# Kernel optimization log

Measured on AMD Instinct MI355X. Metric: run time of the kernel, lower is better.

## Reference

```python
import jax, jax.numpy as jnp
import numpy as np

B, L, C, H, W = 2, 16, 16, 64, 64


def setup_inputs() -> dict:
    key = jax.random.key(0)
    k1, k2 = jax.random.split(key)
    # flows scaled so cumulative normalized-coordinate flows mostly stay in [-1, 1]
    flows = jax.random.normal(k1, (B, L, 2, H, W), dtype=jnp.float32) * 0.05
    images = jax.random.normal(k2, (B, L, C, H, W), dtype=jnp.float32)
    return {"flows": flows, "images": images}


def _bilinear_sample(images, gx, gy):
    # images: [B, Lj, C, H, W]; gx, gy: [B, Li, Lj, H, W] normalized coords in [-1, 1]
    # Replicates torch.nn.functional.grid_sample(mode='bilinear',
    # padding_mode='zeros', align_corners=False).
    Bs, Lj, Cs, Hs, Ws = images.shape
    ix = ((gx + 1.0) * Ws - 1.0) * 0.5  # pixel x coord
    iy = ((gy + 1.0) * Hs - 1.0) * 0.5  # pixel y coord
    x0f = jnp.floor(ix)
    y0f = jnp.floor(iy)
    wx = ix - x0f  # weight toward x0+1 (differentiable w.r.t. flow)
    wy = iy - y0f
    x0 = x0f.astype(jnp.int32)
    y0 = y0f.astype(jnp.int32)
    img_flat = images.reshape(Bs, Lj, Cs, Hs * Ws)

    def gather(xi, yi):
        valid = (xi >= 0) & (xi < Ws) & (yi >= 0) & (yi < Hs)  # [B,Li,Lj,H,W]
        lin = jnp.clip(yi, 0, Hs - 1) * Ws + jnp.clip(xi, 0, Ws - 1)
        lin_t = jnp.transpose(lin, (0, 2, 1, 3, 4))  # [B,Lj,Li,H,W]
        # per (b, j): gather [C, HW] at indices [Li, H, W] -> [C, Li, H, W]
        v = jax.vmap(jax.vmap(lambda im, l: im[:, l]))(img_flat, lin_t)
        v = jnp.transpose(v, (0, 3, 1, 2, 4, 5))  # [B,Li,Lj,C,H,W]
        return v * valid[:, :, :, None, :, :].astype(v.dtype)

    v00 = gather(x0, y0)
    v01 = gather(x0 + 1, y0)
    v10 = gather(x0, y0 + 1)
    v11 = gather(x0 + 1, y0 + 1)
    wX = wx[:, :, :, None, :, :]
    wY = wy[:, :, :, None, :, :]
    return (v00 * (1.0 - wX) * (1.0 - wY) + v01 * wX * (1.0 - wY)
            + v10 * (1.0 - wX) * wY + v11 * wX * wY)


def reference(flows, images):
    Bs, Ls, _, Hs, Ws = flows.shape
    dt = flows.dtype
    cum = jnp.cumsum(flows, axis=1)  # [B,L,2,H,W]
    # rel[b, i, j] = cum[b, i] - cum[b, j]  -> [B,Li,Lj,2,H,W]
    rel = cum[:, :, None] - cum[:, None, :]
    # base sampling grid (pixel centers in normalized coords)
    gx_base = (jnp.arange(Ws, dtype=dt) + 0.5) * (2.0 / Ws) - 1.0  # [W]
    gy_base = (jnp.arange(Hs, dtype=dt) + 0.5) * (2.0 / Hs) - 1.0  # [H]
    gx = gx_base + rel[:, :, :, 0]              # [B,Li,Lj,H,W]
    gy = gy_base[:, None] + rel[:, :, :, 1]     # [B,Li,Lj,H,W]
    gx = jnp.remainder(gx + 1.0, 2.0) - 1.0     # wrap x into [-1, 1)
    warped = _bilinear_sample(images, gx, gy)   # [B,Li,Lj,C,H,W]
    mask = jnp.tril(jnp.ones((Ls, Ls), dtype=dt))
    # causal accumulate over source index j
    return jnp.einsum('bijchw,ij->bichw', warped, mask)
```

## Files before the change

kernel.cpp:

```cpp
#include <hip/hip_runtime.h>
#include <hip/hip_fp16.h>

#define BB 2
#define LL 16
#define CC 16
#define HH 64
#define WW 64
#define HWSZ (HH * WW)

__device__ __forceinline__ float2 cvt2(unsigned int u) {
    __half2 h = *reinterpret_cast<const __half2*>(&u);
    return __half22float2(h);
}

__global__ __launch_bounds__(256) void gsp_prep(
    const float* __restrict__ images,
    uint4* __restrict__ h16)
{
    const int gid  = blockIdx.x * 256 + threadIdx.x;
    const int half = gid & 1;
    const int pix  = (gid >> 1) & (HWSZ - 1);
    const int bl   = gid >> 13;

    const float* src = images + (size_t)(bl * CC + half * 8) * HWSZ + pix;
    unsigned short hs[8];
    #pragma unroll
    for (int m = 0; m < 8; ++m) {
        __half h = __float2half(src[(size_t)m * HWSZ]);
        hs[m] = *reinterpret_cast<unsigned short*>(&h);
    }
    uint4 v;
    v.x = (unsigned)hs[0] | ((unsigned)hs[1] << 16);
    v.y = (unsigned)hs[2] | ((unsigned)hs[3] << 16);
    v.z = (unsigned)hs[4] | ((unsigned)hs[5] << 16);
    v.w = (unsigned)hs[6] | ((unsigned)hs[7] << 16);
    h16[((size_t)bl * HWSZ + pix) * 2 + half] = v;
}

__global__ __launch_bounds__(256) void gsp_main(
    const float* __restrict__ flows,
    const uint4* __restrict__ h16,
    float* __restrict__ out)
{
    const int idx  = blockIdx.x;
    const int xcd  = idx & 7;
    const int k    = idx >> 3;
    const int i    = 15 - (k >> 4);
    const int b    = (k >> 3) & 1;
    const int tile = xcd * 8 + (k & 7);

    const int sub  = threadIdx.x & 3;
    const int half = sub & 1;
    const int xc   = sub >> 1;
    const int px   = tile * 64 + (threadIdx.x >> 2);
    const int h = px >> 6;
    const int w = px & (WW - 1);

    float cx16[LL], cy16[LL];
    {
        const float* fb = flows + (size_t)b * LL * 2 * HWSZ + px;
        #pragma unroll
        for (int l = 0; l < LL; ++l) {
            cx16[l] = fb[(size_t)l * 2 * HWSZ];
            cy16[l] = fb[(size_t)l * 2 * HWSZ + HWSZ];
        }
        #pragma unroll
        for (int l = 1; l < LL; ++l) { cx16[l] += cx16[l - 1]; cy16[l] += cy16[l - 1]; }
    }

    const uint4* h16_b = h16 + (size_t)(b * LL) * HWSZ * 2;

    const float gxb = (w + 0.5f) * (2.0f / WW) - 1.0f;
    const float gyb = (h + 0.5f) * (2.0f / HH) - 1.0f;

    float cix = 0.0f, ciy = 0.0f;
    #pragma unroll
    for (int l = 0; l < LL; ++l) { if (l == i) { cix = cx16[l]; ciy = cy16[l]; } }

    float acc[8];
    #pragma unroll
    for (int m = 0; m < 8; ++m) acc[m] = 0.0f;

    #pragma unroll
    for (int j = 0; j < LL - 1; ++j) {
        if (j < i) {
            float gx = gxb + (cix - cx16[j]);
            float gy = gyb + (ciy - cy16[j]);

            float tt = gx + 1.0f;
            tt = tt - floorf(tt * 0.5f) * 2.0f;
            gx = tt - 1.0f;

            const float ix = ((gx + 1.0f) * WW - 1.0f) * 0.5f;
            const float iy = ((gy + 1.0f) * HH - 1.0f) * 0.5f;
            const float x0f = floorf(ix);
            const float y0f = floorf(iy);
            const float fx = ix - x0f;
            const float fy = iy - y0f;
            const int x0 = (int)x0f;
            const int y0 = (int)y0f;

            const int  xr = x0 + xc;
            const bool vx = (xr >= 0) && (xr < WW);
            const int  cx = min(max(xr, 0), WW - 1);
            const float wx = (xc ? fx : (1.0f - fx)) * (vx ? 1.0f : 0.0f);

            const int y1i = y0 + 1;
            const bool vy0 = (y0 >= 0) && (y0 < HH);
            const bool vy1 = (y1i >= 0) && (y1i < HH);
            const int cy0 = min(max(y0, 0), HH - 1);
            const int cy1 = min(max(y1i, 0), HH - 1);

            const uint4* jb = h16_b + (size_t)j * HWSZ * 2;
            const uint4 v0 = jb[(cy0 * WW + cx) * 2 + half];
            const uint4 v1 = jb[(cy1 * WW + cx) * 2 + half];

            const float w0 = wx * (1.0f - fy) * (vy0 ? 1.0f : 0.0f);
            const float w1 = wx * fy * (vy1 ? 1.0f : 0.0f);

            {
                const float2 p0 = cvt2(v0.x), p1 = cvt2(v0.y);
                const float2 p2 = cvt2(v0.z), p3 = cvt2(v0.w);
                acc[0] += w0 * p0.x;  acc[1] += w0 * p0.y;
                acc[2] += w0 * p1.x;  acc[3] += w0 * p1.y;
                acc[4] += w0 * p2.x;  acc[5] += w0 * p2.y;
                acc[6] += w0 * p3.x;  acc[7] += w0 * p3.y;
            }
            {
                const float2 p0 = cvt2(v1.x), p1 = cvt2(v1.y);
                const float2 p2 = cvt2(v1.z), p3 = cvt2(v1.w);
                acc[0] += w1 * p0.x;  acc[1] += w1 * p0.y;
                acc[2] += w1 * p1.x;  acc[3] += w1 * p1.y;
                acc[4] += w1 * p2.x;  acc[5] += w1 * p2.y;
                acc[6] += w1 * p3.x;  acc[7] += w1 * p3.y;
            }
        }
    }

    #pragma unroll
    for (int m = 0; m < 8; ++m) acc[m] += __shfl_xor(acc[m], 2, 64);

    float s0 = xc ? acc[4] : acc[0];
    float s1 = xc ? acc[5] : acc[1];
    float s2 = xc ? acc[6] : acc[2];
    float s3 = xc ? acc[7] : acc[3];

    {
        const uint2* h2 = (const uint2*)h16;
        const uint2 idv = h2[(((size_t)(b * LL + i) * HWSZ + px) * 2 + half) * 2 + xc];
        const float2 p0 = cvt2(idv.x), p1 = cvt2(idv.y);
        s0 += p0.x; s1 += p0.y; s2 += p1.x; s3 += p1.y;
    }

    const int q = half * 2 + xc;
    float* op = out + ((size_t)(b * LL + i) * CC + q * 4) * HWSZ + px;
    __builtin_nontemporal_store(s0, op + 0 * HWSZ);
    __builtin_nontemporal_store(s1, op + 1 * HWSZ);
    __builtin_nontemporal_store(s2, op + 2 * HWSZ);
    __builtin_nontemporal_store(s3, op + 3 * HWSZ);
}

extern "C" void kernel_launch(void* const* d_in, const int* in_sizes, int n_in,
                              void* d_out, int out_size, void* d_ws, size_t ws_size,
                              hipStream_t stream) {
    const float* flows  = (const float*)d_in[0];
    const float* images = (const float*)d_in[1];
    float* out = (float*)d_out;
    uint4* h16 = (uint4*)d_ws;

    gsp_prep<<<1024, 256, 0, stream>>>(images, h16);

    gsp_main<<<2048, 256, 0, stream>>>(flows, h16, out);
}
```

Before: 75.67 us.

## Precompute cumulative flows in prep kernel and software-pipeline gather loop

The prep kernel gains extra blocks that compute per-pixel cumulative flow sums into an interleaved workspace buffer. The main kernel stages these into swizzled shared memory instead of each thread reloading and summing 32 flow values. The unrolled predicated j-loop becomes a runtime loop that prefetches the next iteration's gathers before accumulating the current one, with launch bounds raised to 5 blocks per CU for occupancy. This trades register arrays for shared memory and a barrier, and adds workspace traffic for the cumulative buffer.

```diff
diff --git a/kernel.cpp b/kernel.cpp
--- a/kernel.cpp
+++ b/kernel.cpp
@@ -15,33 +15,104 @@
 
 __global__ __launch_bounds__(256) void gsp_prep(
     const float* __restrict__ images,
-    uint4* __restrict__ h16)
+    const float* __restrict__ flows,
+    uint4* __restrict__ h16,
+    float4* __restrict__ cum4)
 {
-    const int gid  = blockIdx.x * 256 + threadIdx.x;
-    const int half = gid & 1;
-    const int pix  = (gid >> 1) & (HWSZ - 1);
-    const int bl   = gid >> 13;
-
-    const float* src = images + (size_t)(bl * CC + half * 8) * HWSZ + pix;
-    unsigned short hs[8];
-    #pragma unroll
-    for (int m = 0; m < 8; ++m) {
-        __half h = __float2half(src[(size_t)m * HWSZ]);
-        hs[m] = *reinterpret_cast<unsigned short*>(&h);
-    }
-    uint4 v;
-    v.x = (unsigned)hs[0] | ((unsigned)hs[1] << 16);
-    v.y = (unsigned)hs[2] | ((unsigned)hs[3] << 16);
-    v.z = (unsigned)hs[4] | ((unsigned)hs[5] << 16);
-    v.w = (unsigned)hs[6] | ((unsigned)hs[7] << 16);
-    h16[((size_t)bl * HWSZ + pix) * 2 + half] = v;
-}
-
-__global__ __launch_bounds__(256) void gsp_main(
-    const float* __restrict__ flows,
-    const uint4* __restrict__ h16,
+    if (blockIdx.x < 1024) {
+        const int gid  = blockIdx.x * 256 + threadIdx.x;
+        const int half = gid & 1;
+        const int pix  = (gid >> 1) & (HWSZ - 1);
+        const int bl   = gid >> 13;
+
+        const float* src = images + (size_t)(bl * CC + half * 8) * HWSZ + pix;
+        unsigned short hs[8];
+        #pragma unroll
+        for (int m = 0; m < 8; ++m) {
+            __half h = __float2half(src[(size_t)m * HWSZ]);
+            hs[m] = *reinterpret_cast<unsigned short*>(&h);
+        }
+        uint4 v;
+        v.x = (unsigned)hs[0] | ((unsigned)hs[1] << 16);
+        v.y = (unsigned)hs[2] | ((unsigned)hs[3] << 16);
+        v.z = (unsigned)hs[4] | ((unsigned)hs[5] << 16);
+        v.w = (unsigned)hs[6] | ((unsigned)hs[7] << 16);
+        h16[((size_t)bl * HWSZ + pix) * 2 + half] = v;
+        return;
+    }
+
+    const int u  = (blockIdx.x - 1024) * 256 + threadIdx.x;
+    const int b  = u >> 12;
+    const int px = u & (HWSZ - 1);
+    const float* fb = flows + (size_t)b * LL * 2 * HWSZ + px;
+    float cx = 0.0f, cy = 0.0f;
+    float4 o[8];
+    #pragma unroll
+    for (int l = 0; l < LL; ++l) {
+        cx += fb[(size_t)l * 2 * HWSZ];
+        cy += fb[(size_t)l * 2 * HWSZ + HWSZ];
+        if (l & 1) { o[l >> 1].z = cx; o[l >> 1].w = cy; }
+        else       { o[l >> 1].x = cx; o[l >> 1].y = cy; }
+    }
+    float4* ob = cum4 + ((size_t)b * HWSZ + px) * 8;
+    #pragma unroll
+    for (int k2 = 0; k2 < 8; ++k2) ob[k2] = o[k2];
+}
+
+__device__ __forceinline__ void jstep(
+    float cjx, float cjy, float cix, float ciy,
+    float gxb, float gyb, int xc, int half,
+    const uint4* __restrict__ jb,
+    uint4& v0, uint4& v1, float& w0, float& w1)
+{
+    float gx = gxb + (cix - cjx);
+    float gy = gyb + (ciy - cjy);
+    float tt = gx + 1.0f;
+    tt = tt - floorf(tt * 0.5f) * 2.0f;
+    gx = tt - 1.0f;
+
+    const float ix = ((gx + 1.0f) * WW - 1.0f) * 0.5f;
+    const float iy = ((gy + 1.0f) * HH - 1.0f) * 0.5f;
+    const float x0f = floorf(ix);
+    const float y0f = floorf(iy);
+    const float fx = ix - x0f;
+    const float fy = iy - y0f;
+    const int x0 = (int)x0f;
+    const int y0 = (int)y0f;
+
+    const int  xr = x0 + xc;
+    const bool vx = (xr >= 0) && (xr < WW);
+    const int  cx = min(max(xr, 0), WW - 1);
+    const float wx = (xc ? fx : (1.0f - fx)) * (vx ? 1.0f : 0.0f);
+
+    const int y1i = y0 + 1;
+    const bool vy0 = (y0 >= 0) && (y0 < HH);
+    const bool vy1 = (y1i >= 0) && (y1i < HH);
+    const int cy0 = min(max(y0, 0), HH - 1);
+    const int cy1 = min(max(y1i, 0), HH - 1);
+
+    v0 = jb[(cy0 * WW + cx) * 2 + half];
+    v1 = jb[(cy1 * WW + cx) * 2 + half];
+    w0 = wx * (1.0f - fy) * (vy0 ? 1.0f : 0.0f);
+    w1 = wx * fy * (vy1 ? 1.0f : 0.0f);
+}
+
+__device__ __forceinline__ void accum(const uint4 v, const float wv, float acc[8]) {
+    const float2 p0 = cvt2(v.x), p1 = cvt2(v.y);
+    const float2 p2 = cvt2(v.z), p3 = cvt2(v.w);
+    acc[0] += wv * p0.x;  acc[1] += wv * p0.y;
+    acc[2] += wv * p1.x;  acc[3] += wv * p1.y;
+    acc[4] += wv * p2.x;  acc[5] += wv * p2.y;
+    acc[6] += wv * p3.x;  acc[7] += wv * p3.y;
+}
+
+__global__ __launch_bounds__(256, 5) void gsp_main(
+    const uint4*  __restrict__ h16,
+    const float4* __restrict__ cum4,
     float* __restrict__ out)
 {
+    __shared__ float2 scum[64][16];
+
     const int idx  = blockIdx.x;
     const int xcd  = idx & 7;
     const int k    = idx >> 3;
@@ -52,89 +123,55 @@
     const int sub  = threadIdx.x & 3;
     const int half = sub & 1;
     const int xc   = sub >> 1;
-    const int px   = tile * 64 + (threadIdx.x >> 2);
+    const int pl   = threadIdx.x >> 2;
+    const int px   = tile * 64 + pl;
     const int h = px >> 6;
     const int w = px & (WW - 1);
 
-    float cx16[LL], cy16[LL];
     {
-        const float* fb = flows + (size_t)b * LL * 2 * HWSZ + px;
+        const float4* cb = cum4 + ((size_t)b * HWSZ + tile * 64) * 8;
         #pragma unroll
-        for (int l = 0; l < LL; ++l) {
-            cx16[l] = fb[(size_t)l * 2 * HWSZ];
-            cy16[l] = fb[(size_t)l * 2 * HWSZ + HWSZ];
-        }
-        #pragma unroll
-        for (int l = 1; l < LL; ++l) { cx16[l] += cx16[l - 1]; cy16[l] += cy16[l - 1]; }
-    }
-
-    const uint4* h16_b = h16 + (size_t)(b * LL) * HWSZ * 2;
+        for (int t = 0; t < 2; ++t) {
+            const int g  = threadIdx.x * 2 + t;
+            const float4 v = cb[g];
+            const int pp = g >> 3;
+            const int ll = (g & 7) * 2;
+            scum[pp][(ll + pp) & 15]     = make_float2(v.x, v.y);
+            scum[pp][(ll + 1 + pp) & 15] = make_float2(v.z, v.w);
+        }
+    }
+    __syncthreads();
+
+    const float2 ci = scum[pl][(i + pl) & 15];
+    const float cix = ci.x, ciy = ci.y;
 
     const float gxb = (w + 0.5f) * (2.0f / WW) - 1.0f;
     const float gyb = (h + 0.5f) * (2.0f / HH) - 1.0f;
 
-    float cix = 0.0f, ciy = 0.0f;
-    #pragma unroll
-    for (int l = 0; l < LL; ++l) { if (l == i) { cix = cx16[l]; ciy = cy16[l]; } }
+    const uint4* h16_b = h16 + (size_t)(b * LL) * HWSZ * 2;
 
     float acc[8];
     #pragma unroll
     for (int m = 0; m < 8; ++m) acc[m] = 0.0f;
 
-    #pragma unroll
-    for (int j = 0; j < LL - 1; ++j) {
-        if (j < i) {
-            float gx = gxb + (cix - cx16[j]);
-            float gy = gyb + (ciy - cy16[j]);
-
-            float tt = gx + 1.0f;
-            tt = tt - floorf(tt * 0.5f) * 2.0f;
-            gx = tt - 1.0f;
-
-            const float ix = ((gx + 1.0f) * WW - 1.0f) * 0.5f;
-            const float iy = ((gy + 1.0f) * HH - 1.0f) * 0.5f;
-            const float x0f = floorf(ix);
-            const float y0f = floorf(iy);
-            const float fx = ix - x0f;
-            const float fy = iy - y0f;
-            const int x0 = (int)x0f;
-            const int y0 = (int)y0f;
-
-            const int  xr = x0 + xc;
-            const bool vx = (xr >= 0) && (xr < WW);
-            const int  cx = min(max(xr, 0), WW - 1);
-            const float wx = (xc ? fx : (1.0f - fx)) * (vx ? 1.0f : 0.0f);
-
-            const int y1i = y0 + 1;
-            const bool vy0 = (y0 >= 0) && (y0 < HH);
-            const bool vy1 = (y1i >= 0) && (y1i < HH);
-            const int cy0 = min(max(y0, 0), HH - 1);
-            const int cy1 = min(max(y1i, 0), HH - 1);
-
-            const uint4* jb = h16_b + (size_t)j * HWSZ * 2;
-            const uint4 v0 = jb[(cy0 * WW + cx) * 2 + half];
-            const uint4 v1 = jb[(cy1 * WW + cx) * 2 + half];
-
-            const float w0 = wx * (1.0f - fy) * (vy0 ? 1.0f : 0.0f);
-            const float w1 = wx * fy * (vy1 ? 1.0f : 0.0f);
-
-            {
-                const float2 p0 = cvt2(v0.x), p1 = cvt2(v0.y);
-                const float2 p2 = cvt2(v0.z), p3 = cvt2(v0.w);
-                acc[0] += w0 * p0.x;  acc[1] += w0 * p0.y;
-                acc[2] += w0 * p1.x;  acc[3] += w0 * p1.y;
-                acc[4] += w0 * p2.x;  acc[5] += w0 * p2.y;
-                acc[6] += w0 * p3.x;  acc[7] += w0 * p3.y;
-            }
-            {
-                const float2 p0 = cvt2(v1.x), p1 = cvt2(v1.y);
-                const float2 p2 = cvt2(v1.z), p3 = cvt2(v1.w);
-                acc[0] += w1 * p0.x;  acc[1] += w1 * p0.y;
-                acc[2] += w1 * p1.x;  acc[3] += w1 * p1.y;
-                acc[4] += w1 * p2.x;  acc[5] += w1 * p2.y;
-                acc[6] += w1 * p3.x;  acc[7] += w1 * p3.y;
-            }
-        }
+    if (i > 0) {
+        uint4 v0c, v1c; float w0c, w1c;
+        {
+            const float2 cj = scum[pl][(0 + pl) & 15];
+            jstep(cj.x, cj.y, cix, ciy, gxb, gyb, xc, half,
+                  h16_b, v0c, v1c, w0c, w1c);
+        }
+        for (int j = 1; j < i; ++j) {
+            const float2 cj = scum[pl][(j + pl) & 15];
+            uint4 v0n, v1n; float w0n, w1n;
+            jstep(cj.x, cj.y, cix, ciy, gxb, gyb, xc, half,
+                  h16_b + (size_t)j * HWSZ * 2, v0n, v1n, w0n, w1n);
+            accum(v0c, w0c, acc);
+            accum(v1c, w1c, acc);
+            v0c = v0n; v1c = v1n; w0c = w0n; w1c = w1n;
+        }
+        accum(v0c, w0c, acc);
+        accum(v1c, w1c, acc);
     }
 
     #pragma unroll
@@ -166,9 +203,10 @@
     const float* flows  = (const float*)d_in[0];
     const float* images = (const float*)d_in[1];
     float* out = (float*)d_out;
-    uint4* h16 = (uint4*)d_ws;
-
-    gsp_prep<<<1024, 256, 0, stream>>>(images, h16);
-
-    gsp_main<<<2048, 256, 0, stream>>>(flows, h16, out);
-}
+    uint4*  h16  = (uint4*)d_ws;
+    float4* cum4 = (float4*)((char*)d_ws + (size_t)4 * 1024 * 1024);
+
+    gsp_prep<<<1056, 256, 0, stream>>>(images, flows, h16, cum4);
+
+    gsp_main<<<2048, 256, 0, stream>>>(h16, cum4, out);
+}
```

Result: no change. 76.64 us (+1.3%).
